# Kernel optimization log

Hardware: AMD Instinct MI355X
Metric: run time of the kernel (lower is better)

## Reference

```python
import jax, jax.numpy as jnp
import numpy as np
from jax import lax

SF = 2      # scale_factor
K = 5       # up_kernel
G = 1       # up_group
CC = 64     # compressed_channels
EK = 3      # encoder_kernel


def setup_inputs() -> dict:
    key = jax.random.key(0)
    k1, k2, k3, k4, k5 = jax.random.split(key, 5)
    N, C, H, W = 4, 256, 64, 64
    x = jax.random.normal(k1, (N, C, H, W), dtype=jnp.float32)
    # channel compressor: 1x1 conv (CC, C, 1, 1), xavier-ish init
    Wc = jax.random.normal(k2, (CC, C, 1, 1), dtype=jnp.float32) * (1.0 / np.sqrt(C))
    bc = jnp.zeros((CC,), dtype=jnp.float32)
    # content encoder: 3x3 conv -> K*K*G*SF*SF channels
    enc_out = K * K * G * SF * SF
    We = jax.random.normal(k3, (enc_out, CC, EK, EK), dtype=jnp.float32) * (1.0 / np.sqrt(CC * EK * EK))
    be = jnp.zeros((enc_out,), dtype=jnp.float32)
    return {"x": x, "Wc": Wc, "bc": bc, "We": We, "be": be}


def _carafe_forward(x, Wc, bc, We, be):
    N, C, H, W = x.shape
    k2 = K * K
    # channel compressor (1x1 conv)
    comp = lax.conv_general_dilated(x, Wc, (1, 1), 'VALID') + bc[None, :, None, None]
    # content encoder (3x3 conv, padding 1)
    pad_e = (EK - 1) // 2
    m = lax.conv_general_dilated(comp, We, (1, 1), ((pad_e, pad_e), (pad_e, pad_e))) + be[None, :, None, None]
    # pixel shuffle by SF: (N, Cm*SF^2, H, W) -> (N, Cm, H*SF, W*SF)
    Cm = m.shape[1] // (SF * SF)  # == G * K*K
    m = m.reshape(N, Cm, SF, SF, H, W).transpose(0, 1, 4, 2, 5, 3).reshape(N, Cm, H * SF, W * SF)
    # softmax over kernel dimension
    m = jax.nn.softmax(m.reshape(N, G, k2, H * SF, W * SF), axis=2)
    # unfold features into kxk neighborhoods (same padding): (N, C, k2, H, W)
    pad = (K - 1) // 2
    xp = jnp.pad(x, ((0, 0), (0, 0), (pad, pad), (pad, pad)))
    patches = jnp.stack([xp[:, :, i:i + H, j:j + W] for i in range(K) for j in range(K)], axis=2)
    patches = patches.reshape(N, G, C // G, k2, H, W)
    # reassemble: contract over kernel dim BEFORE duplicating to output res.
    # out[n,g,c,h*SF+i,w*SF+j] = sum_k patches[n,g,c,k,h,w] * mask[n,g,k,h*SF+i,w*SF+j]
    mm = m.reshape(N, G, k2, H, SF, W, SF)
    out = jnp.einsum('ngckhw,ngkhiwj->ngchiwj', patches, mm)
    return out.reshape(N, C, H * SF, W * SF)


def reference(x, Wc, bc, We, be):
    return _carafe_forward(x, Wc, bc, We, be)
```

## Files before the change

kernel.cpp:

```cpp
#include <hip/hip_runtime.h>
#include <hip/hip_bf16.h>


#define COMP_F 0
#define WR_F   1115136
#define LOG_F  1179648
#define WS_NEED 11272192ull
#define CSTR 4356

__global__ void k0_wr(const float* __restrict__ We, float* __restrict__ ws) {
    int tid = blockIdx.x * blockDim.x + threadIdx.x;
    if (tid >= 4 * 64 * 9 * 25) return;
    int k  = tid % 25;
    int q  = (tid / 25) % 9;
    int cc = (tid / 225) % 64;
    int ij = tid / 14400;
    ws[WR_F + (((size_t)(ij * 64 + cc) * 9) + q) * 28 + k] =
        We[(size_t)(4 * k + ij) * 576 + cc * 9 + q];
}

__global__ __launch_bounds__(64) void k1_comp(const float* __restrict__ x,
                                              const float* __restrict__ Wc,
                                              const float* __restrict__ bc,
                                              float* __restrict__ ws) {
    int b   = blockIdx.x;
    int pw  = b & 255;
    int ccg = b >> 8;
    int n = pw >> 6, h = pw & 63, w = threadIdx.x;
    int cc0 = ccg * 8;

    float acc[8];
#pragma unroll
    for (int u = 0; u < 8; ++u) acc[u] = 0.f;

    const float* xp = x + (size_t)n * 256 * 4096 + h * 64 + w;
#pragma unroll 4
    for (int c = 0; c < 256; ++c) {
        float xv = xp[(size_t)c * 4096];
#pragma unroll
        for (int u = 0; u < 8; ++u)
            acc[u] += xv * Wc[(cc0 + u) * 256 + c];
    }

    float* compb = ws + COMP_F + (size_t)(n * 64 + cc0) * CSTR;
#pragma unroll
    for (int u = 0; u < 8; ++u) {
        float* cb_ = compb + (size_t)u * CSTR;
        cb_[(h + 1) * 66 + (w + 1)] = acc[u] + bc[cc0 + u];
        if (w < 2) cb_[(h + 1) * 66 + (w ? 65 : 0)] = 0.f;
        if (h == 0)  { cb_[w] = 0.f;           if (w < 2) cb_[64 + w] = 0.f; }
        if (h == 63) { cb_[65 * 66 + w] = 0.f; if (w < 2) cb_[65 * 66 + 64 + w] = 0.f; }
    }
}

template <int K0, int KR>
__device__ void enc_body(const float* __restrict__ compn, const float* __restrict__ wrij,
                         const float* __restrict__ be, float* __restrict__ logits,
                         float* __restrict__ WsL, int n, int th, int tw, int ij) {
    int lane = threadIdx.x;
    int py = lane >> 3, pxx = lane & 7;
    int h = th * 8 + py, w = tw * 8 + pxx;

    float acc[KR];
#pragma unroll
    for (int kk = 0; kk < KR; ++kk) acc[kk] = be[4 * (K0 + kk) + ij];

    for (int cb = 0; cb < 64; cb += 16) {
        for (int p = lane; p < 144; p += 64) {
            int c_ = p / 9, q = p % 9;
            const float* src = wrij + (size_t)(cb + c_) * 252 + q * 28 + K0;
            float* dst = WsL + p * 16;
#pragma unroll
            for (int kk = 0; kk < KR; ++kk) dst[kk] = src[kk];
        }
        __syncthreads();
#pragma unroll 2
        for (int c_ = 0; c_ < 16; ++c_) {
            const float* cp = compn + (size_t)(cb + c_) * CSTR + h * 66 + w;
            float cv[9];
#pragma unroll
            for (int dy = 0; dy < 3; ++dy)
#pragma unroll
                for (int dx = 0; dx < 3; ++dx)
                    cv[dy * 3 + dx] = cp[dy * 66 + dx];
#pragma unroll
            for (int q = 0; q < 9; ++q) {
                float v = cv[q];
                const float* row = WsL + (c_ * 9 + q) * 16;
#pragma unroll
                for (int kk = 0; kk < KR; ++kk) acc[kk] += v * row[kk];
            }
        }
        __syncthreads();
    }

    float* lp = logits + (size_t)(n * 4096 + h * 64 + w) * 100 + ij;
#pragma unroll
    for (int kk = 0; kk < KR; ++kk) lp[4 * (K0 + kk)] = acc[kk];
}

__global__ __launch_bounds__(64) void k2_enc(const float* __restrict__ be,
                                             float* __restrict__ ws) {
    __shared__ float WsL[144 * 16];
    int b    = blockIdx.x;
    int tile = b & 255;
    int ij   = (b >> 8) & 3;
    int kh   = b >> 10;
    int n = tile >> 6, th = (tile >> 3) & 7, tw = tile & 7;

    const float* compn = ws + COMP_F + (size_t)n * 64 * CSTR;
    const float* wrij  = ws + WR_F + (size_t)ij * 64 * 252;
    float* logits = ws + LOG_F;
    if (kh == 0) enc_body<0, 13>(compn, wrij, be, logits, WsL, n, th, tw, ij);
    else         enc_body<13, 12>(compn, wrij, be, logits, WsL, n, th, tw, ij);
}

__global__ __launch_bounds__(256) void k3_out(const float* __restrict__ x,
                                              const float* __restrict__ ws,
                                              float* __restrict__ out) {
    __shared__ float xt[16 * 400];
    int b      = blockIdx.x;
    int tile   = b & 63;
    int cchunk = b >> 6;
    int n = tile >> 4, ty0 = ((tile >> 2) & 3) * 16, tx0 = (tile & 3) * 16;
    int c0 = cchunk * 16;

    const float* xn = x + (size_t)(n * 256 + c0) * 4096;
    for (int e = threadIdx.x; e < 16 * 400; e += 256) {
        int c = e / 400, r = (e % 400) / 20, q = e % 20;
        int hh = ty0 + r - 2, ww = tx0 + q - 2;
        float v = 0.f;
        if (hh >= 0 && hh < 64 && ww >= 0 && ww < 64) v = xn[(size_t)c * 4096 + hh * 64 + ww];
        xt[e] = v;
    }

    int py = threadIdx.x >> 4, pxx = threadIdx.x & 15;
    int h = ty0 + py, w = tx0 + pxx;
    const float* lp = ws + LOG_F + (size_t)(n * 4096 + h * 64 + w) * 100;
    float4 mk[25];
#pragma unroll
    for (int t = 0; t < 25; ++t) mk[t] = ((const float4*)lp)[t];

    float4 mx = mk[0];
#pragma unroll
    for (int t = 1; t < 25; ++t) {
        mx.x = fmaxf(mx.x, mk[t].x); mx.y = fmaxf(mx.y, mk[t].y);
        mx.z = fmaxf(mx.z, mk[t].z); mx.w = fmaxf(mx.w, mk[t].w);
    }
    float4 sm = {0.f, 0.f, 0.f, 0.f};
#pragma unroll
    for (int t = 0; t < 25; ++t) {
        mk[t].x = __expf(mk[t].x - mx.x); sm.x += mk[t].x;
        mk[t].y = __expf(mk[t].y - mx.y); sm.y += mk[t].y;
        mk[t].z = __expf(mk[t].z - mx.z); sm.z += mk[t].z;
        mk[t].w = __expf(mk[t].w - mx.w); sm.w += mk[t].w;
    }
    float4 iv = {1.f / sm.x, 1.f / sm.y, 1.f / sm.z, 1.f / sm.w};
#pragma unroll
    for (int t = 0; t < 25; ++t) {
        mk[t].x *= iv.x; mk[t].y *= iv.y; mk[t].z *= iv.z; mk[t].w *= iv.w;
    }
    __syncthreads();

    for (int c = 0; c < 16; ++c) {
        const float* xc = xt + c * 400 + py * 20 + pxx;
        float a0 = 0.f, a1 = 0.f, a2 = 0.f, a3 = 0.f;
#pragma unroll
        for (int t = 0; t < 25; ++t) {
            float v = xc[(t / 5) * 20 + (t % 5)];
            a0 += v * mk[t].x; a1 += v * mk[t].y;
            a2 += v * mk[t].z; a3 += v * mk[t].w;
        }
        size_t ob = (((size_t)(n * 256 + c0 + c) * 128) + 2 * h) * 128 + 2 * w;
        float2 r0 = {a0, a1}, r1 = {a2, a3};
        *(float2*)(out + ob)       = r0;
        *(float2*)(out + ob + 128) = r1;
    }
}

__global__ __launch_bounds__(256) void k_fused(const float* __restrict__ x,
                                               const float* __restrict__ Wc,
                                               const float* __restrict__ bc,
                                               const float* __restrict__ We,
                                               const float* __restrict__ be,
                                               float* __restrict__ out) {
    __shared__ float compS[64 * 101];
    int n = blockIdx.x >> 6, tile = blockIdx.x & 63;
    int ty0 = (tile >> 3) * 8, tx0 = (tile & 7) * 8;
    const float* xn = x + (size_t)n * 256 * 4096;
    {
        int pa = threadIdx.x & 127;
        int ga = __builtin_amdgcn_readfirstlane(threadIdx.x >> 7);
        bool act = pa < 100;
        int ah = ty0 + pa / 10 - 1, aw = tx0 + pa % 10 - 1;
        bool inb = act && ah >= 0 && ah < 64 && aw >= 0 && aw < 64;
        int xoff = ah * 64 + aw;
        float acc[32];
#pragma unroll
        for (int i = 0; i < 32; ++i) acc[i] = 0.f;
        for (int c = 0; c < 256; ++c) {
            float xv = inb ? xn[(size_t)c * 4096 + xoff] : 0.f;
#pragma unroll
            for (int i = 0; i < 32; ++i) acc[i] += xv * Wc[(ga * 32 + i) * 256 + c];
        }
        if (act)
#pragma unroll
            for (int i = 0; i < 32; ++i) {
                int cc = ga * 32 + i;
                compS[cc * 101 + pa] = inb ? acc[i] + bc[cc] : 0.f;
            }
    }
    __syncthreads();
    int px = threadIdx.x & 63;
    int ij = __builtin_amdgcn_readfirstlane(threadIdx.x >> 6);
    int py = px >> 3, pxx = px & 7;
    int h = ty0 + py, w = tx0 + pxx;
    float m[25];
#pragma unroll
    for (int k = 0; k < 25; ++k) m[k] = be[4 * k + ij];
    for (int cc = 0; cc < 64; ++cc) {
        float cv[9];
#pragma unroll
        for (int dy = 0; dy < 3; ++dy)
#pragma unroll
            for (int dx = 0; dx < 3; ++dx)
                cv[dy * 3 + dx] = compS[cc * 101 + (py + dy) * 10 + (pxx + dx)];
        int base = cc * 9;
#pragma unroll
        for (int k = 0; k < 25; ++k) {
            int eb = (4 * k + ij) * 576 + base;
            float s = 0.f;
#pragma unroll
            for (int qb = 0; qb < 9; ++qb) s += cv[qb] * We[eb + qb];
            m[k] += s;
        }
    }
    float mxv = m[0];
#pragma unroll
    for (int k = 1; k < 25; ++k) mxv = fmaxf(mxv, m[k]);
    float ss = 0.f;
#pragma unroll
    for (int k = 0; k < 25; ++k) { m[k] = __expf(m[k] - mxv); ss += m[k]; }
    float inv = 1.f / ss;
#pragma unroll
    for (int k = 0; k < 25; ++k) m[k] *= inv;
    int offs[25];
    unsigned vm = 0;
#pragma unroll
    for (int t = 0; t < 25; ++t) {
        int hh = h + t / 5 - 2, ww = w + t % 5 - 2;
        bool v = hh >= 0 && hh < 64 && ww >= 0 && ww < 64;
        offs[t] = v ? hh * 64 + ww : 0;
        if (v) vm |= 1u << t;
    }
    size_t outp = ((size_t)n * 256 * 128 + (2 * h + (ij >> 1))) * 128 + (2 * w + (ij & 1));
    for (int c = 0; c < 256; ++c) {
        const float* xc = xn + (size_t)c * 4096;
        float sum = 0.f;
#pragma unroll
        for (int t = 0; t < 25; ++t) {
            float v = ((vm >> t) & 1u) ? xc[offs[t]] : 0.f;
            sum += v * m[t];
        }
        out[outp + (size_t)c * 16384] = sum;
    }
}

extern "C" void kernel_launch(void* const* d_in, const int* in_sizes, int n_in,
                              void* d_out, int out_size, void* d_ws, size_t ws_size,
                              hipStream_t stream) {
    const float* x  = (const float*)d_in[0];
    const float* Wc = (const float*)d_in[1];
    const float* bc = (const float*)d_in[2];
    const float* We = (const float*)d_in[3];
    const float* be = (const float*)d_in[4];
    float* out = (float*)d_out;

    if (ws_size >= WS_NEED && d_ws != nullptr) {
        float* ws = (float*)d_ws;
        hipLaunchKernelGGL(k0_wr,   dim3(225),  dim3(256), 0, stream, We, ws);
        hipLaunchKernelGGL(k1_comp, dim3(2048), dim3(64),  0, stream, x, Wc, bc, ws);
        hipLaunchKernelGGL(k2_enc,  dim3(2048), dim3(64),  0, stream, be, ws);
        hipLaunchKernelGGL(k3_out,  dim3(1024), dim3(256), 0, stream, x, ws, out);
    } else {
        hipLaunchKernelGGL(k_fused, dim3(256),  dim3(256), 0, stream,
                           x, Wc, bc, We, be, out);
    }
}
```

Measured before the change: 209.8 us.

## Stage compressed tile in LDS and share it across four encoder waves

The content-encoder kernel now uses 256-thread blocks. Each block loads a 10x10x64 halo tile of the compressed features into shared memory once, and its four waves, one per sub-pixel index ij, all read from that tile. The output channels are split into three chunks instead of two, so each thread holds fewer accumulators. Each wave stages its own weight slice, so the per-chunk __syncthreads calls become a wave-local LDS wait. This cuts redundant global reads of the compressed map and block-wide barriers, at the cost of more shared memory per block (about 53 KB) and relying on wave-lockstep behaviour for correctness.

```diff
diff --git a/kernel.cpp b/kernel.cpp
--- a/kernel.cpp
+++ b/kernel.cpp
@@ -54,65 +54,76 @@
 }
 
 template <int K0, int KR>
-__device__ void enc_body(const float* __restrict__ compn, const float* __restrict__ wrij,
-                         const float* __restrict__ be, float* __restrict__ logits,
-                         float* __restrict__ WsL, int n, int th, int tw, int ij) {
-    int lane = threadIdx.x;
-    int py = lane >> 3, pxx = lane & 7;
-    int h = th * 8 + py, w = tw * 8 + pxx;
+__device__ void enc_body(const float* __restrict__ wr, const float* __restrict__ be,
+                         float* __restrict__ logits, const float* __restrict__ compn,
+                         float* compT, float* Wt, int n, int th, int tw) {
+    const int tid  = threadIdx.x;
+    const int lane = tid & 63;
+    const int ij   = tid >> 6;
+    const int py = lane >> 3, pxx = lane & 7;
+    const int h0 = th * 8, w0 = tw * 8;
+
+    for (int e = tid; e < 6400; e += 256) {
+        int c = e / 100, rq = e % 100;
+        compT[e] = compn[(size_t)c * CSTR + (h0 + rq / 10) * 66 + (w0 + rq % 10)];
+    }
+    __syncthreads();
 
     float acc[KR];
 #pragma unroll
     for (int kk = 0; kk < KR; ++kk) acc[kk] = be[4 * (K0 + kk) + ij];
 
+    float* wslice = Wt + ij * (144 * 12);
+    const float* wsrc = wr + (size_t)ij * 64 * 252;
+
     for (int cb = 0; cb < 64; cb += 16) {
-        for (int p = lane; p < 144; p += 64) {
-            int c_ = p / 9, q = p % 9;
-            const float* src = wrij + (size_t)(cb + c_) * 252 + q * 28 + K0;
-            float* dst = WsL + p * 16;
-#pragma unroll
-            for (int kk = 0; kk < KR; ++kk) dst[kk] = src[kk];
-        }
-        __syncthreads();
+        for (int rowi = lane; rowi < 144; rowi += 64) {
+            const float* s = wsrc + (size_t)(cb + rowi / 9) * 252 + (rowi % 9) * 28 + K0;
+            float* d = wslice + rowi * 12;
+#pragma unroll
+            for (int kk = 0; kk < KR; ++kk) d[kk] = s[kk];
+        }
+        asm volatile("s_waitcnt lgkmcnt(0)" ::: "memory");
+
 #pragma unroll 2
         for (int c_ = 0; c_ < 16; ++c_) {
-            const float* cp = compn + (size_t)(cb + c_) * CSTR + h * 66 + w;
+            const float* cp = compT + (cb + c_) * 100 + py * 10 + pxx;
             float cv[9];
 #pragma unroll
             for (int dy = 0; dy < 3; ++dy)
 #pragma unroll
                 for (int dx = 0; dx < 3; ++dx)
-                    cv[dy * 3 + dx] = cp[dy * 66 + dx];
+                    cv[dy * 3 + dx] = cp[dy * 10 + dx];
+            const float* wrow = wslice + c_ * 108;
 #pragma unroll
             for (int q = 0; q < 9; ++q) {
                 float v = cv[q];
-                const float* row = WsL + (c_ * 9 + q) * 16;
-#pragma unroll
-                for (int kk = 0; kk < KR; ++kk) acc[kk] += v * row[kk];
+#pragma unroll
+                for (int kk = 0; kk < KR; ++kk)
+                    acc[kk] += v * wrow[q * 12 + kk];
             }
         }
-        __syncthreads();
-    }
-
-    float* lp = logits + (size_t)(n * 4096 + h * 64 + w) * 100 + ij;
+    }
+
+    float* lp = logits + ((size_t)(n * 4096 + (h0 + py) * 64 + (w0 + pxx))) * 100 + ij;
 #pragma unroll
     for (int kk = 0; kk < KR; ++kk) lp[4 * (K0 + kk)] = acc[kk];
 }
 
-__global__ __launch_bounds__(64) void k2_enc(const float* __restrict__ be,
-                                             float* __restrict__ ws) {
-    __shared__ float WsL[144 * 16];
+__global__ __launch_bounds__(256, 3) void k2_enc(const float* __restrict__ be,
+                                                 float* __restrict__ ws) {
+    __shared__ __align__(16) float compT[6400];
+    __shared__ __align__(16) float Wt[4 * 144 * 12];
     int b    = blockIdx.x;
     int tile = b & 255;
-    int ij   = (b >> 8) & 3;
-    int kh   = b >> 10;
+    int kt   = b >> 8;
     int n = tile >> 6, th = (tile >> 3) & 7, tw = tile & 7;
-
-    const float* compn = ws + COMP_F + (size_t)n * 64 * CSTR;
-    const float* wrij  = ws + WR_F + (size_t)ij * 64 * 252;
-    float* logits = ws + LOG_F;
-    if (kh == 0) enc_body<0, 13>(compn, wrij, be, logits, WsL, n, th, tw, ij);
-    else         enc_body<13, 12>(compn, wrij, be, logits, WsL, n, th, tw, ij);
+    const float* compn  = ws + COMP_F + (size_t)n * 64 * CSTR;
+    const float* wr     = ws + WR_F;
+    float*       logits = ws + LOG_F;
+    if (kt == 0)      enc_body<0, 9>(wr, be, logits, compn, compT, Wt, n, th, tw);
+    else if (kt == 1) enc_body<9, 8>(wr, be, logits, compn, compT, Wt, n, th, tw);
+    else              enc_body<17, 8>(wr, be, logits, compn, compT, Wt, n, th, tw);
 }
 
 __global__ __launch_bounds__(256) void k3_out(const float* __restrict__ x,
@@ -280,7 +291,7 @@
         float* ws = (float*)d_ws;
         hipLaunchKernelGGL(k0_wr,   dim3(225),  dim3(256), 0, stream, We, ws);
         hipLaunchKernelGGL(k1_comp, dim3(2048), dim3(64),  0, stream, x, Wc, bc, ws);
-        hipLaunchKernelGGL(k2_enc,  dim3(2048), dim3(64),  0, stream, be, ws);
+        hipLaunchKernelGGL(k2_enc,  dim3(768),  dim3(256), 0, stream, be, ws);
         hipLaunchKernelGGL(k3_out,  dim3(1024), dim3(256), 0, stream, x, ws, out);
     } else {
         hipLaunchKernelGGL(k_fused, dim3(256),  dim3(256), 0, stream,
```

New measurement: 207.6 us. Within noise of the previous version (-1.0%).

## Stage compressed tile in LDS and split encoder across four subpixel waves

Applied to the files above, without the earlier changes.

The content-encoder kernel now loads each 10x10 halo tile of all 64 compressed channels into shared memory once per block. Four wavefronts, one per subpixel offset, share that tile, and each computes 5 logits per pixel. The weights are re-laid out per (subpixel, kernel-group) slice and read directly from global memory with wave-uniform addresses, so the per-chunk LDS weight staging and its barriers go away. This cuts redundant global reads of the compressed feature map, at the cost of 30KB of LDS per block and more blocks each doing less work.

```diff
diff --git a/kernel.cpp b/kernel.cpp
--- a/kernel.cpp
+++ b/kernel.cpp
@@ -10,13 +10,14 @@
 
 __global__ void k0_wr(const float* __restrict__ We, float* __restrict__ ws) {
     int tid = blockIdx.x * blockDim.x + threadIdx.x;
-    if (tid >= 4 * 64 * 9 * 25) return;
-    int k  = tid % 25;
-    int q  = (tid / 25) % 9;
-    int cc = (tid / 225) % 64;
+    if (tid >= 4 * 5 * 64 * 45) return;
+    int kk = tid % 5;
+    int q  = (tid / 5) % 9;
+    int cc = (tid / 45) % 64;
+    int kt = (tid / 2880) % 5;
     int ij = tid / 14400;
-    ws[WR_F + (((size_t)(ij * 64 + cc) * 9) + q) * 28 + k] =
-        We[(size_t)(4 * k + ij) * 576 + cc * 9 + q];
+    ws[WR_F + (size_t)(((ij * 5 + kt) * 64 + cc)) * 48 + q * 5 + kk] =
+        We[(size_t)(4 * (kt * 5 + kk) + ij) * 576 + cc * 9 + q];
 }
 
 __global__ __launch_bounds__(64) void k1_comp(const float* __restrict__ x,
@@ -53,66 +54,57 @@
     }
 }
 
-template <int K0, int KR>
-__device__ void enc_body(const float* __restrict__ compn, const float* __restrict__ wrij,
-                         const float* __restrict__ be, float* __restrict__ logits,
-                         float* __restrict__ WsL, int n, int th, int tw, int ij) {
-    int lane = threadIdx.x;
-    int py = lane >> 3, pxx = lane & 7;
-    int h = th * 8 + py, w = tw * 8 + pxx;
-
-    float acc[KR];
-#pragma unroll
-    for (int kk = 0; kk < KR; ++kk) acc[kk] = be[4 * (K0 + kk) + ij];
-
-    for (int cb = 0; cb < 64; cb += 16) {
-        for (int p = lane; p < 144; p += 64) {
-            int c_ = p / 9, q = p % 9;
-            const float* src = wrij + (size_t)(cb + c_) * 252 + q * 28 + K0;
-            float* dst = WsL + p * 16;
-#pragma unroll
-            for (int kk = 0; kk < KR; ++kk) dst[kk] = src[kk];
-        }
-        __syncthreads();
-#pragma unroll 2
-        for (int c_ = 0; c_ < 16; ++c_) {
-            const float* cp = compn + (size_t)(cb + c_) * CSTR + h * 66 + w;
-            float cv[9];
-#pragma unroll
-            for (int dy = 0; dy < 3; ++dy)
-#pragma unroll
-                for (int dx = 0; dx < 3; ++dx)
-                    cv[dy * 3 + dx] = cp[dy * 66 + dx];
-#pragma unroll
-            for (int q = 0; q < 9; ++q) {
-                float v = cv[q];
-                const float* row = WsL + (c_ * 9 + q) * 16;
-#pragma unroll
-                for (int kk = 0; kk < KR; ++kk) acc[kk] += v * row[kk];
-            }
-        }
-        __syncthreads();
-    }
-
-    float* lp = logits + (size_t)(n * 4096 + h * 64 + w) * 100 + ij;
-#pragma unroll
-    for (int kk = 0; kk < KR; ++kk) lp[4 * (K0 + kk)] = acc[kk];
-}
-
-__global__ __launch_bounds__(64) void k2_enc(const float* __restrict__ be,
-                                             float* __restrict__ ws) {
-    __shared__ float WsL[144 * 16];
+__global__ __launch_bounds__(256, 5) void k2_enc(const float* __restrict__ be,
+                                                 float* __restrict__ ws) {
+    __shared__ __align__(16) float compT[64 * 120];
     int b    = blockIdx.x;
     int tile = b & 255;
-    int ij   = (b >> 8) & 3;
-    int kh   = b >> 10;
+    int kt   = b >> 8;
     int n = tile >> 6, th = (tile >> 3) & 7, tw = tile & 7;
+    int h0 = th * 8, w0 = tw * 8;
+    int tid = threadIdx.x;
 
     const float* compn = ws + COMP_F + (size_t)n * 64 * CSTR;
-    const float* wrij  = ws + WR_F + (size_t)ij * 64 * 252;
-    float* logits = ws + LOG_F;
-    if (kh == 0) enc_body<0, 13>(compn, wrij, be, logits, WsL, n, th, tw, ij);
-    else         enc_body<13, 12>(compn, wrij, be, logits, WsL, n, th, tw, ij);
+    for (int e = tid; e < 6400; e += 256) {
+        int c = e / 100, rq = e % 100, r = rq / 10, q = rq % 10;
+        compT[c * 120 + r * 12 + q] =
+            compn[(size_t)c * CSTR + (h0 + r) * 66 + (w0 + q)];
+    }
+    __syncthreads();
+
+    int lane = tid & 63;
+    int ij   = __builtin_amdgcn_readfirstlane(tid >> 6);
+    int py = lane >> 3, pxx = lane & 7;
+
+    const float* wb = ws + WR_F + (size_t)((ij * 5 + kt) * 64) * 48;
+
+    float acc[5];
+#pragma unroll
+    for (int kk = 0; kk < 5; ++kk) acc[kk] = be[4 * (kt * 5 + kk) + ij];
+
+#pragma unroll 2
+    for (int c = 0; c < 64; ++c) {
+        const float* cp = compT + c * 120 + py * 12 + pxx;
+        float cv[9];
+#pragma unroll
+        for (int dy = 0; dy < 3; ++dy)
+#pragma unroll
+            for (int dx = 0; dx < 3; ++dx)
+                cv[dy * 3 + dx] = cp[dy * 12 + dx];
+        const float* w = wb + c * 48;
+#pragma unroll
+        for (int q = 0; q < 9; ++q) {
+            float v = cv[q];
+#pragma unroll
+            for (int kk = 0; kk < 5; ++kk)
+                acc[kk] += v * w[q * 5 + kk];
+        }
+    }
+
+    float* lp = ws + LOG_F +
+                (size_t)(n * 4096 + (h0 + py) * 64 + (w0 + pxx)) * 100 + ij;
+#pragma unroll
+    for (int kk = 0; kk < 5; ++kk) lp[4 * (kt * 5 + kk)] = acc[kk];
 }
 
 __global__ __launch_bounds__(256) void k3_out(const float* __restrict__ x,
@@ -278,9 +270,9 @@
 
     if (ws_size >= WS_NEED && d_ws != nullptr) {
         float* ws = (float*)d_ws;
-        hipLaunchKernelGGL(k0_wr,   dim3(225),  dim3(256), 0, stream, We, ws);
+        hipLaunchKernelGGL(k0_wr,   dim3(226),  dim3(256), 0, stream, We, ws);
         hipLaunchKernelGGL(k1_comp, dim3(2048), dim3(64),  0, stream, x, Wc, bc, ws);
-        hipLaunchKernelGGL(k2_enc,  dim3(2048), dim3(64),  0, stream, be, ws);
+        hipLaunchKernelGGL(k2_enc,  dim3(1280), dim3(256), 0, stream, be, ws);
         hipLaunchKernelGGL(k3_out,  dim3(1024), dim3(256), 0, stream, x, ws, out);
     } else {
         hipLaunchKernelGGL(k_fused, dim3(256),  dim3(256), 0, stream,
```

Result: faster. 195.8 us (-6.7%).
